# Performance work log

Hardware: AMD Instinct MI355X
Metric: run time of the kernel (lower is better)

## Reference

```python
import jax, jax.numpy as jnp
import numpy as np

NUM_SEGMENTS = 4096  # number of episodes (len(batch['lengths']))


def setup_inputs() -> dict:
    key = jax.random.key(0)
    k1, k2, k3, k4, k5 = jax.random.split(key, 5)
    N = 65536
    emb_a = jax.random.normal(k1, (N, 256), dtype=jnp.float32)
    emb_b = jax.random.normal(k2, (N, 256), dtype=jnp.float32)
    segment_ids = jnp.sort(jax.random.randint(k3, (N,), 0, NUM_SEGMENTS, dtype=jnp.int32))
    W = jax.random.normal(k4, (32, 512), dtype=jnp.float32) * (1.0 / np.sqrt(512.0))
    b = jax.random.normal(k5, (32,), dtype=jnp.float32) * 0.01
    return {"emb_a": emb_a, "emb_b": emb_b, "segment_ids": segment_ids, "W": W, "b": b}


def reference(emb_a, emb_b, segment_ids, W, b):
    # torch.cat([embeds[key] for key in project_keys], dim=1)
    combined = jnp.concatenate([emb_a, emb_b], axis=1)  # [N, 512]
    # split_with_sizes + per-split mean + stack == segment mean
    sums = jax.ops.segment_sum(combined, segment_ids, num_segments=NUM_SEGMENTS)  # [S, 512]
    counts = jax.ops.segment_sum(jnp.ones((combined.shape[0],), combined.dtype),
                                 segment_ids, num_segments=NUM_SEGMENTS)  # [S]
    pooled = sums / jnp.maximum(counts, 1.0)[:, None]  # [S, 512]
    # dropout is identity in eval mode; final nn.Linear
    return pooled @ W.T + b  # [S, 32]
```

## Files before the change

kernel.cpp:

```cpp
#include <hip/hip_runtime.h>

#define NSEG 4096

__global__ __launch_bounds__(128, 8) void fused_pool_proj_kernel(
    const float* __restrict__ emb_a,
    const float* __restrict__ emb_b,
    const int*   __restrict__ seg,
    const float* __restrict__ W,
    const float* __restrict__ bias,
    float*       __restrict__ out,
    int nrows)
{
    const int s    = blockIdx.x;
    const int t    = threadIdx.x;
    const int wave = t >> 6;
    const int lane = t & 63;

    __shared__ int   bounds[2];
    __shared__ float pooled[512];
    __shared__ float sh_out[32];

    if (t < 2) {
        int target = s + t;
        int lo = 0, hi = nrows;
        while (lo < hi) {
            int mid = (lo + hi) >> 1;
            if (seg[mid] < target) lo = mid + 1; else hi = mid;
        }
        bounds[t] = lo;
    }
    __syncthreads();
    const int start = bounds[0];
    const int end   = bounds[1];
    const int cnt   = end - start;

    const float*  base = (wave == 0) ? emb_a : emb_b;
    const float4* src  = reinterpret_cast<const float4*>(base) + lane;

    float4 a0 = make_float4(0.f,0.f,0.f,0.f);
    float4 a1 = make_float4(0.f,0.f,0.f,0.f);
    float4 a2 = make_float4(0.f,0.f,0.f,0.f);
    float4 a3 = make_float4(0.f,0.f,0.f,0.f);

    int r = start;
    for (; r + 4 <= end; r += 4) {
        float4 v0 = src[(size_t)(r + 0) * 64];
        float4 v1 = src[(size_t)(r + 1) * 64];
        float4 v2 = src[(size_t)(r + 2) * 64];
        float4 v3 = src[(size_t)(r + 3) * 64];
        a0.x += v0.x; a0.y += v0.y; a0.z += v0.z; a0.w += v0.w;
        a1.x += v1.x; a1.y += v1.y; a1.z += v1.z; a1.w += v1.w;
        a2.x += v2.x; a2.y += v2.y; a2.z += v2.z; a2.w += v2.w;
        a3.x += v3.x; a3.y += v3.y; a3.z += v3.z; a3.w += v3.w;
    }
    for (; r < end; ++r) {
        float4 v = src[(size_t)r * 64];
        a0.x += v.x; a0.y += v.y; a0.z += v.z; a0.w += v.w;
    }

    const float inv = 1.0f / (float)max(cnt, 1);
    float4 acc;
    acc.x = (a0.x + a1.x + a2.x + a3.x) * inv;
    acc.y = (a0.y + a1.y + a2.y + a3.y) * inv;
    acc.z = (a0.z + a1.z + a2.z + a3.z) * inv;
    acc.w = (a0.w + a1.w + a2.w + a3.w) * inv;

    *reinterpret_cast<float4*>(pooled + (wave << 8) + (lane << 2)) = acc;
    __syncthreads();

    const float4* pool4 = reinterpret_cast<const float4*>(pooled);
    const float4  p0 = pool4[lane];
    const float4  p1 = pool4[64 + lane];

    #pragma unroll 4
    for (int jj = 0; jj < 16; ++jj) {
        const int j = (wave << 4) + jj;
        const float4* wrow = reinterpret_cast<const float4*>(W + j * 512);
        const float4  w0 = wrow[lane];
        const float4  w1 = wrow[64 + lane];
        float v = p0.x*w0.x + p0.y*w0.y + p0.z*w0.z + p0.w*w0.w
                + p1.x*w1.x + p1.y*w1.y + p1.z*w1.z + p1.w*w1.w;
        v += __shfl_xor(v, 1);
        v += __shfl_xor(v, 2);
        v += __shfl_xor(v, 4);
        v += __shfl_xor(v, 8);
        v += __shfl_xor(v, 16);
        v += __shfl_xor(v, 32);
        if (lane == 0) sh_out[j] = v + bias[j];
    }
    __syncthreads();

    if (t < 32) out[s * 32 + t] = sh_out[t];
}

extern "C" void kernel_launch(void* const* d_in, const int* in_sizes, int n_in,
                              void* d_out, int out_size, void* d_ws, size_t ws_size,
                              hipStream_t stream) {
    const float* emb_a = (const float*)d_in[0];
    const float* emb_b = (const float*)d_in[1];
    const int*   seg   = (const int*)d_in[2];
    const float* W     = (const float*)d_in[3];
    const float* bias  = (const float*)d_in[4];
    float*       out   = (float*)d_out;
    const int nrows = in_sizes[2];

    fused_pool_proj_kernel<<<NSEG, 128, 0, stream>>>(emb_a, emb_b, seg, W, bias, out, nrows);
}
```

Before: 37.96 us.

## Precompute segment bounds in a scatter kernel and split rows across four waves

A separate kernel now writes segment start offsets into workspace by scattering at each boundary of the sorted ids, replacing the per-block binary search. The main kernel uses 256 threads, with each segment's rows split in half across wave pairs and the partial sums combined in shared memory. That doubles memory-level parallelism per segment. It also halves the projection rows per wave. The cost is an extra kernel launch, and the old path is kept as a fallback when workspace is too small.

```diff
diff --git a/kernel.cpp b/kernel.cpp
--- a/kernel.cpp
+++ b/kernel.cpp
@@ -2,7 +2,110 @@
 
 #define NSEG 4096
 
-__global__ __launch_bounds__(128, 8) void fused_pool_proj_kernel(
+__global__ __launch_bounds__(256) void scatter_bounds_kernel(
+    const int* __restrict__ seg, int* __restrict__ bounds, int nrows)
+{
+    const int i = blockIdx.x * 256 + threadIdx.x;
+    if (i >= nrows) return;
+    const int cur  = seg[i];
+    const int prev = (i == 0) ? -1 : seg[i - 1];
+    for (int s = prev + 1; s <= cur; ++s) bounds[s] = i;
+    if (i == nrows - 1) {
+        for (int s = cur + 1; s <= NSEG; ++s) bounds[s] = nrows;
+    }
+}
+
+__global__ __launch_bounds__(256, 4) void fused_pool_proj_kernel(
+    const float* __restrict__ emb_a,
+    const float* __restrict__ emb_b,
+    const int*   __restrict__ bounds,
+    const float* __restrict__ W,
+    const float* __restrict__ bias,
+    float*       __restrict__ out)
+{
+    const int s    = blockIdx.x;
+    const int t    = threadIdx.x;
+    const int wave = t >> 6;
+    const int lane = t & 63;
+
+    __shared__ float pooled[1024];
+    __shared__ float sh_out[32];
+
+    const int start = bounds[s];
+    const int end   = bounds[s + 1];
+    const int cnt   = end - start;
+    const int mid   = start + (cnt >> 1);
+
+    const int r0 = (wave >> 1) ? mid : start;
+    const int r1 = (wave >> 1) ? end : mid;
+
+    const float*  base = (wave & 1) ? emb_b : emb_a;
+    const float4* src  = reinterpret_cast<const float4*>(base) + lane;
+
+    float4 a0 = make_float4(0.f,0.f,0.f,0.f);
+    float4 a1 = make_float4(0.f,0.f,0.f,0.f);
+    float4 a2 = make_float4(0.f,0.f,0.f,0.f);
+    float4 a3 = make_float4(0.f,0.f,0.f,0.f);
+
+    int r = r0;
+    for (; r + 4 <= r1; r += 4) {
+        float4 v0 = src[(size_t)(r + 0) * 64];
+        float4 v1 = src[(size_t)(r + 1) * 64];
+        float4 v2 = src[(size_t)(r + 2) * 64];
+        float4 v3 = src[(size_t)(r + 3) * 64];
+        a0.x += v0.x; a0.y += v0.y; a0.z += v0.z; a0.w += v0.w;
+        a1.x += v1.x; a1.y += v1.y; a1.z += v1.z; a1.w += v1.w;
+        a2.x += v2.x; a2.y += v2.y; a2.z += v2.z; a2.w += v2.w;
+        a3.x += v3.x; a3.y += v3.y; a3.z += v3.z; a3.w += v3.w;
+    }
+    for (; r < r1; ++r) {
+        float4 v = src[(size_t)r * 64];
+        a0.x += v.x; a0.y += v.y; a0.z += v.z; a0.w += v.w;
+    }
+
+    float4 acc;
+    acc.x = a0.x + a1.x + a2.x + a3.x;
+    acc.y = a0.y + a1.y + a2.y + a3.y;
+    acc.z = a0.z + a1.z + a2.z + a3.z;
+    acc.w = a0.w + a1.w + a2.w + a3.w;
+
+    *reinterpret_cast<float4*>(pooled + (wave << 8) + (lane << 2)) = acc;
+    __syncthreads();
+
+    const float inv = 1.0f / (float)max(cnt, 1);
+    const float4* pool4 = reinterpret_cast<const float4*>(pooled);
+    const float4 qa0 = pool4[lane];
+    const float4 qa1 = pool4[128 + lane];
+    const float4 qb0 = pool4[64 + lane];
+    const float4 qb1 = pool4[192 + lane];
+    float4 p0, p1;
+    p0.x = (qa0.x + qa1.x) * inv;  p0.y = (qa0.y + qa1.y) * inv;
+    p0.z = (qa0.z + qa1.z) * inv;  p0.w = (qa0.w + qa1.w) * inv;
+    p1.x = (qb0.x + qb1.x) * inv;  p1.y = (qb0.y + qb1.y) * inv;
+    p1.z = (qb0.z + qb1.z) * inv;  p1.w = (qb0.w + qb1.w) * inv;
+
+    #pragma unroll 4
+    for (int jj = 0; jj < 8; ++jj) {
+        const int j = (wave << 3) + jj;
+        const float4* wrow = reinterpret_cast<const float4*>(W + j * 512);
+        const float4  w0 = wrow[lane];
+        const float4  w1 = wrow[64 + lane];
+        float v = p0.x*w0.x + p0.y*w0.y + p0.z*w0.z + p0.w*w0.w
+                + p1.x*w1.x + p1.y*w1.y + p1.z*w1.z + p1.w*w1.w;
+        v += __shfl_xor(v, 1);
+        v += __shfl_xor(v, 2);
+        v += __shfl_xor(v, 4);
+        v += __shfl_xor(v, 8);
+        v += __shfl_xor(v, 16);
+        v += __shfl_xor(v, 32);
+        if (lane == 0) sh_out[j] = v + bias[j];
+    }
+    __syncthreads();
+
+    if (t < 32) out[s * 32 + t] = sh_out[t];
+}
+
+__global__ __launch_bounds__(128, 8) void fused_fallback_kernel(
     const float* __restrict__ emb_a,
     const float* __restrict__ emb_b,
     const int*   __restrict__ seg,
@@ -11,37 +114,28 @@
     float*       __restrict__ out,
     int nrows)
 {
-    const int s    = blockIdx.x;
-    const int t    = threadIdx.x;
+    const int s = blockIdx.x;
+    const int t = threadIdx.x;
     const int wave = t >> 6;
     const int lane = t & 63;
-
     __shared__ int   bounds[2];
     __shared__ float pooled[512];
     __shared__ float sh_out[32];
-
     if (t < 2) {
         int target = s + t;
         int lo = 0, hi = nrows;
-        while (lo < hi) {
-            int mid = (lo + hi) >> 1;
-            if (seg[mid] < target) lo = mid + 1; else hi = mid;
-        }
+        while (lo < hi) { int mid = (lo + hi) >> 1; if (seg[mid] < target) lo = mid + 1; else hi = mid; }
         bounds[t] = lo;
     }
     __syncthreads();
-    const int start = bounds[0];
-    const int end   = bounds[1];
-    const int cnt   = end - start;
-
+    const int start = bounds[0], end = bounds[1];
+    const int cnt = end - start;
     const float*  base = (wave == 0) ? emb_a : emb_b;
     const float4* src  = reinterpret_cast<const float4*>(base) + lane;
-
     float4 a0 = make_float4(0.f,0.f,0.f,0.f);
     float4 a1 = make_float4(0.f,0.f,0.f,0.f);
     float4 a2 = make_float4(0.f,0.f,0.f,0.f);
     float4 a3 = make_float4(0.f,0.f,0.f,0.f);
-
     int r = start;
     for (; r + 4 <= end; r += 4) {
         float4 v0 = src[(size_t)(r + 0) * 64];
@@ -57,21 +151,17 @@
         float4 v = src[(size_t)r * 64];
         a0.x += v.x; a0.y += v.y; a0.z += v.z; a0.w += v.w;
     }
-
     const float inv = 1.0f / (float)max(cnt, 1);
     float4 acc;
     acc.x = (a0.x + a1.x + a2.x + a3.x) * inv;
     acc.y = (a0.y + a1.y + a2.y + a3.y) * inv;
     acc.z = (a0.z + a1.z + a2.z + a3.z) * inv;
     acc.w = (a0.w + a1.w + a2.w + a3.w) * inv;
-
     *reinterpret_cast<float4*>(pooled + (wave << 8) + (lane << 2)) = acc;
     __syncthreads();
-
     const float4* pool4 = reinterpret_cast<const float4*>(pooled);
     const float4  p0 = pool4[lane];
     const float4  p1 = pool4[64 + lane];
-
     #pragma unroll 4
     for (int jj = 0; jj < 16; ++jj) {
         const int j = (wave << 4) + jj;
@@ -89,7 +179,6 @@
         if (lane == 0) sh_out[j] = v + bias[j];
     }
     __syncthreads();
-
     if (t < 32) out[s * 32 + t] = sh_out[t];
 }
 
@@ -104,5 +193,12 @@
     float*       out   = (float*)d_out;
     const int nrows = in_sizes[2];
 
-    fused_pool_proj_kernel<<<NSEG, 128, 0, stream>>>(emb_a, emb_b, seg, W, bias, out, nrows);
-}
+    const size_t need = (size_t)(NSEG + 1) * sizeof(int);
+    if (ws_size >= need) {
+        int* bounds = (int*)d_ws;
+        scatter_bounds_kernel<<<(nrows + 255) / 256, 256, 0, stream>>>(seg, bounds, nrows);
+        fused_pool_proj_kernel<<<NSEG, 256, 0, stream>>>(emb_a, emb_b, bounds, W, bias, out);
+    } else {
+        fused_fallback_kernel<<<NSEG, 128, 0, stream>>>(emb_a, emb_b, seg, W, bias, out, nrows);
+    }
+}
```

After: 38.10 us. No clear change (+0.4%).

## Split fused pool-projection into setup, pooling, and projection kernels

Applied to the files above, without the earlier changes.

Replaces the single fused kernel with three launches. The first builds segment boundaries by scanning adjacent ids and transposes W. The second pools two segments per block with a deeper unroll and writes the pooled rows to workspace. The third runs the projection over 16 segments per block using the transposed W. This drops the per-block binary search and the shuffle reductions, but it adds two kernel launches and an 8 MB round trip of pooled data through global memory. The original fused kernel is kept as a fallback when workspace is too small.

```diff
diff --git a/kernel.cpp b/kernel.cpp
--- a/kernel.cpp
+++ b/kernel.cpp
@@ -2,7 +2,117 @@
 
 #define NSEG 4096
 
-__global__ __launch_bounds__(128, 8) void fused_pool_proj_kernel(
+__device__ __forceinline__ void acc4(float4& a, const float4 v) {
+    a.x += v.x; a.y += v.y; a.z += v.z; a.w += v.w;
+}
+
+__global__ __launch_bounds__(256) void setup_kernel(
+    const int*   __restrict__ seg,
+    const float* __restrict__ W,
+    int*         __restrict__ bounds,
+    float*       __restrict__ Wt,
+    int nrows)
+{
+    const int i = blockIdx.x * 256 + threadIdx.x;
+    if (i < 512 * 32) {
+        const int d = i >> 5, j = i & 31;
+        Wt[i] = W[j * 512 + d];
+    }
+    if (i >= nrows) return;
+    const int cur  = seg[i];
+    const int prev = (i == 0) ? -1 : seg[i - 1];
+    for (int s = prev + 1; s <= cur; ++s) bounds[s] = i;
+    if (i == nrows - 1) {
+        for (int s = cur + 1; s <= NSEG; ++s) bounds[s] = nrows;
+    }
+}
+
+__global__ __launch_bounds__(256, 8) void pool_kernel(
+    const float* __restrict__ emb_a,
+    const float* __restrict__ emb_b,
+    const int*   __restrict__ bounds,
+    float*       __restrict__ pooled)
+{
+    const int t    = threadIdx.x;
+    const int wave = t >> 6;
+    const int lane = t & 63;
+    const int s    = (blockIdx.x << 1) + (wave >> 1);
+
+    const int start = bounds[s];
+    const int end   = bounds[s + 1];
+    const int cnt   = end - start;
+
+    const float*  base = (wave & 1) ? emb_b : emb_a;
+    const float4* src  = reinterpret_cast<const float4*>(base) + lane;
+
+    float4 a0{0,0,0,0}, a1{0,0,0,0}, a2{0,0,0,0}, a3{0,0,0,0};
+
+    int r = start;
+    for (; r + 8 <= end; r += 8) {
+        float4 v0 = src[(size_t)(r+0)*64];
+        float4 v1 = src[(size_t)(r+1)*64];
+        float4 v2 = src[(size_t)(r+2)*64];
+        float4 v3 = src[(size_t)(r+3)*64];
+        float4 v4 = src[(size_t)(r+4)*64];
+        float4 v5 = src[(size_t)(r+5)*64];
+        float4 v6 = src[(size_t)(r+6)*64];
+        float4 v7 = src[(size_t)(r+7)*64];
+        acc4(a0, v0); acc4(a1, v1); acc4(a2, v2); acc4(a3, v3);
+        acc4(a0, v4); acc4(a1, v5); acc4(a2, v6); acc4(a3, v7);
+    }
+    for (; r + 4 <= end; r += 4) {
+        float4 v0 = src[(size_t)(r+0)*64];
+        float4 v1 = src[(size_t)(r+1)*64];
+        float4 v2 = src[(size_t)(r+2)*64];
+        float4 v3 = src[(size_t)(r+3)*64];
+        acc4(a0, v0); acc4(a1, v1); acc4(a2, v2); acc4(a3, v3);
+    }
+    for (; r < end; ++r) acc4(a0, src[(size_t)r * 64]);
+
+    const float inv = 1.0f / (float)max(cnt, 1);
+    float4 acc;
+    acc.x = (a0.x + a1.x + a2.x + a3.x) * inv;
+    acc.y = (a0.y + a1.y + a2.y + a3.y) * inv;
+    acc.z = (a0.z + a1.z + a2.z + a3.z) * inv;
+    acc.w = (a0.w + a1.w + a2.w + a3.w) * inv;
+
+    *reinterpret_cast<float4*>(pooled + (size_t)s * 512 + ((wave & 1) << 8) + (lane << 2)) = acc;
+}
+
+__global__ __launch_bounds__(128) void proj_kernel(
+    const float* __restrict__ pooled,
+    const float* __restrict__ Wt,
+    const float* __restrict__ bias,
+    float*       __restrict__ out)
+{
+    const int t   = threadIdx.x;
+    const int seg = blockIdx.x * 16 + (t >> 3);
+    const int j4  = t & 7;
+
+    const float4* P  = reinterpret_cast<const float4*>(pooled + (size_t)seg * 512);
+    const float4* WT = reinterpret_cast<const float4*>(Wt) + j4;
+
+    float4 acc{0,0,0,0};
+    #pragma unroll 4
+    for (int d4 = 0; d4 < 128; ++d4) {
+        const float4 p  = P[d4];
+        const float4 w0 = WT[(size_t)(4*d4 + 0) * 8];
+        const float4 w1 = WT[(size_t)(4*d4 + 1) * 8];
+        const float4 w2 = WT[(size_t)(4*d4 + 2) * 8];
+        const float4 w3 = WT[(size_t)(4*d4 + 3) * 8];
+        acc.x += p.x*w0.x + p.y*w1.x + p.z*w2.x + p.w*w3.x;
+        acc.y += p.x*w0.y + p.y*w1.y + p.z*w2.y + p.w*w3.y;
+        acc.z += p.x*w0.z + p.y*w1.z + p.z*w2.z + p.w*w3.z;
+        acc.w += p.x*w0.w + p.y*w1.w + p.z*w2.w + p.w*w3.w;
+    }
+    const float4 bb = reinterpret_cast<const float4*>(bias)[j4];
+    float4 o;
+    o.x = acc.x + bb.x; o.y = acc.y + bb.y;
+    o.z = acc.z + bb.z; o.w = acc.w + bb.w;
+    reinterpret_cast<float4*>(out + (size_t)seg * 32)[j4] = o;
+}
+
+__global__ __launch_bounds__(128, 8) void fused_fallback_kernel(
     const float* __restrict__ emb_a,
     const float* __restrict__ emb_b,
     const int*   __restrict__ seg,
@@ -11,67 +121,45 @@
     float*       __restrict__ out,
     int nrows)
 {
-    const int s    = blockIdx.x;
-    const int t    = threadIdx.x;
+    const int s = blockIdx.x;
+    const int t = threadIdx.x;
     const int wave = t >> 6;
     const int lane = t & 63;
-
-    __shared__ int   bounds[2];
+    __shared__ int   bnd[2];
     __shared__ float pooled[512];
     __shared__ float sh_out[32];
-
     if (t < 2) {
         int target = s + t;
         int lo = 0, hi = nrows;
-        while (lo < hi) {
-            int mid = (lo + hi) >> 1;
-            if (seg[mid] < target) lo = mid + 1; else hi = mid;
-        }
-        bounds[t] = lo;
+        while (lo < hi) { int mid = (lo + hi) >> 1; if (seg[mid] < target) lo = mid + 1; else hi = mid; }
+        bnd[t] = lo;
     }
     __syncthreads();
-    const int start = bounds[0];
-    const int end   = bounds[1];
-    const int cnt   = end - start;
-
+    const int start = bnd[0], end = bnd[1];
+    const int cnt = end - start;
     const float*  base = (wave == 0) ? emb_a : emb_b;
     const float4* src  = reinterpret_cast<const float4*>(base) + lane;
-
-    float4 a0 = make_float4(0.f,0.f,0.f,0.f);
-    float4 a1 = make_float4(0.f,0.f,0.f,0.f);
-    float4 a2 = make_float4(0.f,0.f,0.f,0.f);
-    float4 a3 = make_float4(0.f,0.f,0.f,0.f);
-
+    float4 a0{0,0,0,0}, a1{0,0,0,0}, a2{0,0,0,0}, a3{0,0,0,0};
     int r = start;
     for (; r + 4 <= end; r += 4) {
-        float4 v0 = src[(size_t)(r + 0) * 64];
-        float4 v1 = src[(size_t)(r + 1) * 64];
-        float4 v2 = src[(size_t)(r + 2) * 64];
-        float4 v3 = src[(size_t)(r + 3) * 64];
-        a0.x += v0.x; a0.y += v0.y; a0.z += v0.z; a0.w += v0.w;
-        a1.x += v1.x; a1.y += v1.y; a1.z += v1.z; a1.w += v1.w;
-        a2.x += v2.x; a2.y += v2.y; a2.z += v2.z; a2.w += v2.w;
-        a3.x += v3.x; a3.y += v3.y; a3.z += v3.z; a3.w += v3.w;
-    }
-    for (; r < end; ++r) {
-        float4 v = src[(size_t)r * 64];
-        a0.x += v.x; a0.y += v.y; a0.z += v.z; a0.w += v.w;
-    }
-
+        float4 v0 = src[(size_t)(r+0)*64];
+        float4 v1 = src[(size_t)(r+1)*64];
+        float4 v2 = src[(size_t)(r+2)*64];
+        float4 v3 = src[(size_t)(r+3)*64];
+        acc4(a0, v0); acc4(a1, v1); acc4(a2, v2); acc4(a3, v3);
+    }
+    for (; r < end; ++r) acc4(a0, src[(size_t)r * 64]);
     const float inv = 1.0f / (float)max(cnt, 1);
     float4 acc;
     acc.x = (a0.x + a1.x + a2.x + a3.x) * inv;
     acc.y = (a0.y + a1.y + a2.y + a3.y) * inv;
     acc.z = (a0.z + a1.z + a2.z + a3.z) * inv;
     acc.w = (a0.w + a1.w + a2.w + a3.w) * inv;
-
     *reinterpret_cast<float4*>(pooled + (wave << 8) + (lane << 2)) = acc;
     __syncthreads();
-
     const float4* pool4 = reinterpret_cast<const float4*>(pooled);
     const float4  p0 = pool4[lane];
     const float4  p1 = pool4[64 + lane];
-
     #pragma unroll 4
     for (int jj = 0; jj < 16; ++jj) {
         const int j = (wave << 4) + jj;
@@ -89,7 +177,6 @@
         if (lane == 0) sh_out[j] = v + bias[j];
     }
     __syncthreads();
-
     if (t < 32) out[s * 32 + t] = sh_out[t];
 }
 
@@ -104,5 +191,18 @@
     float*       out   = (float*)d_out;
     const int nrows = in_sizes[2];
 
-    fused_pool_proj_kernel<<<NSEG, 128, 0, stream>>>(emb_a, emb_b, seg, W, bias, out, nrows);
-}
+    const size_t OFF_WT     = 32768;
+    const size_t OFF_POOLED = 98304;
+    const size_t need       = OFF_POOLED + (size_t)NSEG * 512 * sizeof(float);
+
+    if (ws_size >= need) {
+        int*   bounds = (int*)d_ws;
+        float* Wt     = (float*)((char*)d_ws + OFF_WT);
+        float* pooled = (float*)((char*)d_ws + OFF_POOLED);
+        setup_kernel<<<(nrows + 255) / 256, 256, 0, stream>>>(seg, W, bounds, Wt, nrows);
+        pool_kernel<<<NSEG / 2, 256, 0, stream>>>(emb_a, emb_b, bounds, pooled);
+        proj_kernel<<<NSEG / 16, 128, 0, stream>>>(pooled, Wt, bias, out);
+    } else {
+        fused_fallback_kernel<<<NSEG, 128, 0, stream>>>(emb_a, emb_b, seg, W, bias, out, nrows);
+    }
+}
```

New measurement: 58.78 us. 54.9% more time.

## Split each segment's rows across four waves and unroll loads by eight

Applied to the files above, without the earlier changes.

The block grows from 128 to 256 threads. Each segment's rows are split into two halves handled by separate waves, so four waves each accumulate one half of one embedding table. Partial sums are combined in shared memory before the mean and projection, and the projection loop now gives each wave 8 output rows instead of 16. The main load loop is unrolled to 8 rows to keep more memory requests in flight, at the cost of more registers and an extra shared-memory reduction.

```diff
diff --git a/kernel.cpp b/kernel.cpp
--- a/kernel.cpp
+++ b/kernel.cpp
@@ -2,7 +2,11 @@
 
 #define NSEG 4096
 
-__global__ __launch_bounds__(128, 8) void fused_pool_proj_kernel(
+__device__ __forceinline__ void acc4(float4& a, const float4 v) {
+    a.x += v.x; a.y += v.y; a.z += v.z; a.w += v.w;
+}
+
+__global__ __launch_bounds__(256, 8) void fused_kernel(
     const float* __restrict__ emb_a,
     const float* __restrict__ emb_b,
     const int*   __restrict__ seg,
@@ -16,8 +20,8 @@
     const int wave = t >> 6;
     const int lane = t & 63;
 
-    __shared__ int   bounds[2];
-    __shared__ float pooled[512];
+    __shared__ int   bnd[2];
+    __shared__ float pooled[1024];
     __shared__ float sh_out[32];
 
     if (t < 2) {
@@ -27,54 +31,65 @@
             int mid = (lo + hi) >> 1;
             if (seg[mid] < target) lo = mid + 1; else hi = mid;
         }
-        bounds[t] = lo;
+        bnd[t] = lo;
     }
     __syncthreads();
-    const int start = bounds[0];
-    const int end   = bounds[1];
+    const int start = bnd[0];
+    const int end   = bnd[1];
     const int cnt   = end - start;
+    const int mid   = start + (cnt >> 1);
+    const int r0    = (wave >> 1) ? mid : start;
+    const int r1    = (wave >> 1) ? end : mid;
 
-    const float*  base = (wave == 0) ? emb_a : emb_b;
+    const float*  base = (wave & 1) ? emb_b : emb_a;
     const float4* src  = reinterpret_cast<const float4*>(base) + lane;
 
-    float4 a0 = make_float4(0.f,0.f,0.f,0.f);
-    float4 a1 = make_float4(0.f,0.f,0.f,0.f);
-    float4 a2 = make_float4(0.f,0.f,0.f,0.f);
-    float4 a3 = make_float4(0.f,0.f,0.f,0.f);
+    float4 a0{0,0,0,0}, a1{0,0,0,0}, a2{0,0,0,0}, a3{0,0,0,0};
+    int r = r0;
+    for (; r + 8 <= r1; r += 8) {
+        float4 v0 = src[(size_t)(r+0)*64];
+        float4 v1 = src[(size_t)(r+1)*64];
+        float4 v2 = src[(size_t)(r+2)*64];
+        float4 v3 = src[(size_t)(r+3)*64];
+        float4 v4 = src[(size_t)(r+4)*64];
+        float4 v5 = src[(size_t)(r+5)*64];
+        float4 v6 = src[(size_t)(r+6)*64];
+        float4 v7 = src[(size_t)(r+7)*64];
+        acc4(a0, v0); acc4(a1, v1); acc4(a2, v2); acc4(a3, v3);
+        acc4(a0, v4); acc4(a1, v5); acc4(a2, v6); acc4(a3, v7);
+    }
+    for (; r + 4 <= r1; r += 4) {
+        float4 v0 = src[(size_t)(r+0)*64];
+        float4 v1 = src[(size_t)(r+1)*64];
+        float4 v2 = src[(size_t)(r+2)*64];
+        float4 v3 = src[(size_t)(r+3)*64];
+        acc4(a0, v0); acc4(a1, v1); acc4(a2, v2); acc4(a3, v3);
+    }
+    for (; r < r1; ++r) acc4(a0, src[(size_t)r * 64]);
 
-    int r = start;
-    for (; r + 4 <= end; r += 4) {
-        float4 v0 = src[(size_t)(r + 0) * 64];
-        float4 v1 = src[(size_t)(r + 1) * 64];
-        float4 v2 = src[(size_t)(r + 2) * 64];
-        float4 v3 = src[(size_t)(r + 3) * 64];
-        a0.x += v0.x; a0.y += v0.y; a0.z += v0.z; a0.w += v0.w;
-        a1.x += v1.x; a1.y += v1.y; a1.z += v1.z; a1.w += v1.w;
-        a2.x += v2.x; a2.y += v2.y; a2.z += v2.z; a2.w += v2.w;
-        a3.x += v3.x; a3.y += v3.y; a3.z += v3.z; a3.w += v3.w;
-    }
-    for (; r < end; ++r) {
-        float4 v = src[(size_t)r * 64];
-        a0.x += v.x; a0.y += v.y; a0.z += v.z; a0.w += v.w;
-    }
-
-    const float inv = 1.0f / (float)max(cnt, 1);
     float4 acc;
-    acc.x = (a0.x + a1.x + a2.x + a3.x) * inv;
-    acc.y = (a0.y + a1.y + a2.y + a3.y) * inv;
-    acc.z = (a0.z + a1.z + a2.z + a3.z) * inv;
-    acc.w = (a0.w + a1.w + a2.w + a3.w) * inv;
-
+    acc.x = a0.x + a1.x + a2.x + a3.x;
+    acc.y = a0.y + a1.y + a2.y + a3.y;
+    acc.z = a0.z + a1.z + a2.z + a3.z;
+    acc.w = a0.w + a1.w + a2.w + a3.w;
     *reinterpret_cast<float4*>(pooled + (wave << 8) + (lane << 2)) = acc;
     __syncthreads();
 
+    const float inv = 1.0f / (float)max(cnt, 1);
     const float4* pool4 = reinterpret_cast<const float4*>(pooled);
-    const float4  p0 = pool4[lane];
-    const float4  p1 = pool4[64 + lane];
+    const float4 qa0 = pool4[lane];
+    const float4 qb0 = pool4[64 + lane];
+    const float4 qa1 = pool4[128 + lane];
+    const float4 qb1 = pool4[192 + lane];
+    float4 p0, p1;
+    p0.x = (qa0.x + qa1.x) * inv;  p0.y = (qa0.y + qa1.y) * inv;
+    p0.z = (qa0.z + qa1.z) * inv;  p0.w = (qa0.w + qa1.w) * inv;
+    p1.x = (qb0.x + qb1.x) * inv;  p1.y = (qb0.y + qb1.y) * inv;
+    p1.z = (qb0.z + qb1.z) * inv;  p1.w = (qb0.w + qb1.w) * inv;
 
     #pragma unroll 4
-    for (int jj = 0; jj < 16; ++jj) {
-        const int j = (wave << 4) + jj;
+    for (int jj = 0; jj < 8; ++jj) {
+        const int j = (wave << 3) + jj;
         const float4* wrow = reinterpret_cast<const float4*>(W + j * 512);
         const float4  w0 = wrow[lane];
         const float4  w1 = wrow[64 + lane];
@@ -104,5 +119,5 @@
     float*       out   = (float*)d_out;
     const int nrows = in_sizes[2];
 
-    fused_pool_proj_kernel<<<NSEG, 128, 0, stream>>>(emb_a, emb_b, seg, W, bias, out, nrows);
+    fused_kernel<<<NSEG, 256, 0, stream>>>(emb_a, emb_b, seg, W, bias, out, nrows);
 }
```

Result: slower. 39.60 us (+4.3%).
